# Performance work log

Measured on AMD Instinct MI355X. Metric: run time of the kernel, lower is better.

## Reference

```python
import jax, jax.numpy as jnp
import numpy as np

EMBED = 1024
HEADS = 16
DK = EMBED // HEADS


def setup_inputs() -> dict:
    key = jax.random.key(0)
    ks = jax.random.split(key, 6)
    B, S = 2, 2048
    scale = 1.0 / np.sqrt(EMBED)
    x = jax.random.normal(ks[0], (B, S, EMBED), dtype=jnp.float32)
    Wq = jax.random.normal(ks[1], (EMBED, EMBED), dtype=jnp.float32) * scale
    Wk = jax.random.normal(ks[2], (EMBED, EMBED), dtype=jnp.float32) * scale
    Wv = jax.random.normal(ks[3], (EMBED, EMBED), dtype=jnp.float32) * scale
    Wo = jax.random.normal(ks[4], (EMBED, EMBED), dtype=jnp.float32) * scale
    qw = jnp.zeros((HEADS, 1), dtype=jnp.float32)  # quantum_weight, init quantum_scale=0
    return {"x": x, "Wq": Wq, "Wk": Wk, "Wv": Wv, "Wo": Wo, "qw": qw}


def reference(x, Wq, Wk, Wv, Wo, qw):
    B, S, E = x.shape
    # nn.Linear with no bias: y = x @ W.T; split heads -> [B,H,S,Dk]
    def proj(W):
        return (x @ W.T).reshape(B, S, HEADS, DK).transpose(0, 2, 1, 3)
    q, k, v = proj(Wq), proj(Wk), proj(Wv)
    scores = jnp.einsum('bhsd,bhtd->bhst', q, k) / np.sqrt(DK)
    attn = jax.nn.softmax(scores, axis=-1)  # dropout in eval mode: identity
    classical = jnp.einsum('bhst,bhtd->bhsd', attn, v)
    w = jax.nn.sigmoid(qw)[:, :, None]  # [H,1,1] per-head mixing weight
    out = w * jnp.sin(classical) + (1.0 - w) * classical
    out = out.transpose(0, 2, 1, 3).reshape(B, S, E)
    return out @ Wo.T
```

## Files before the change

kernel.cpp:

```cpp
#include <hip/hip_runtime.h>
#include <math.h>

constexpr int Ec  = 1024;
constexpr int Hc  = 16;
constexpr int DKc = 64;
constexpr int Bc  = 2;
constexpr int Sc  = 2048;
constexpr int Mc  = Bc * Sc;

typedef _Float16 half8 __attribute__((ext_vector_type(8)));
typedef _Float16 half4 __attribute__((ext_vector_type(4)));
typedef float    floatx4 __attribute__((ext_vector_type(4)));

#define MFMA16(a, b, c) __builtin_amdgcn_mfma_f32_16x16x32_f16(a, b, c, 0, 0, 0)

__device__ __forceinline__ void async_lds16(const _Float16* g, _Float16* l)
{
    __builtin_amdgcn_global_load_lds(
        (const __attribute__((address_space(1))) unsigned int*)g,
        (__attribute__((address_space(3))) unsigned int*)l, 16, 0, 0);
}

__global__ __launch_bounds__(256)
void convert_to_h(const float4* __restrict__ x,
                  const float4* __restrict__ wq,
                  const float4* __restrict__ wk,
                  const float4* __restrict__ wv,
                  const float4* __restrict__ wo,
                  half4* __restrict__ dst)
{
    const int i = blockIdx.x * 256 + threadIdx.x;
    const float4* src; int off;
    if      (i < 1048576) { src = x;  off = i; }
    else if (i < 1310720) { src = wq; off = i - 1048576; }
    else if (i < 1572864) { src = wk; off = i - 1310720; }
    else if (i < 1835008) { src = wv; off = i - 1572864; }
    else                  { src = wo; off = i - 1835008; }
    const float4 v = src[off];
    half4 o;
    o.x = (_Float16)v.x; o.y = (_Float16)v.y;
    o.z = (_Float16)v.z; o.w = (_Float16)v.w;
    dst[i] = o;
}

__device__ __forceinline__ void mfma_gemm_core(const _Float16* __restrict__ A,
                                               const _Float16* __restrict__ Bw,
                                               int m0, int n0,
                                               _Float16* As, _Float16* Bs,
                                               floatx4 acc[4][4])
{
    const int tid  = threadIdx.x;
    const int wave = tid >> 6, lane = tid & 63;
    const int l16  = lane & 15, quad = lane >> 4;
    const int wrow = (wave >> 1) * 64, wcol = (wave & 1) * 64;

    const int srow = wave * 32 + (lane >> 2);
    const int kseg = (lane & 3) * 8;
    const _Float16* ga = A  + (size_t)(m0 + srow) * Ec + kseg;
    const _Float16* gb = Bw + (size_t)(n0 + srow) * Ec + kseg;
    _Float16* lA = As + wave * 1024;
    _Float16* lB = Bs + wave * 1024;

    for (int kt = 0; kt < Ec; kt += 32) {
        async_lds16(ga,             lA);
        async_lds16(ga + 16 * Ec,   lA + 512);
        async_lds16(gb,             lB);
        async_lds16(gb + 16 * Ec,   lB + 512);
        ga += 32; gb += 32;
        __syncthreads();

        half8 af[4], bf[4];
#pragma unroll
        for (int i = 0; i < 4; ++i)
            af[i] = *(const half8*)&As[(wrow + i * 16 + l16) * 32 + quad * 8];
#pragma unroll
        for (int j = 0; j < 4; ++j)
            bf[j] = *(const half8*)&Bs[(wcol + j * 16 + l16) * 32 + quad * 8];
#pragma unroll
        for (int i = 0; i < 4; ++i)
#pragma unroll
            for (int j = 0; j < 4; ++j)
                acc[i][j] = MFMA16(af[i], bf[j], acc[i][j]);
        __syncthreads();
    }
}

__global__ __launch_bounds__(256)
void gemm_qkv_mfma(const _Float16* __restrict__ xh,
                   const _Float16* __restrict__ wqh,
                   const _Float16* __restrict__ wkh,
                   const _Float16* __restrict__ wvh,
                   _Float16* __restrict__ Qh,
                   _Float16* __restrict__ Kh,
                   _Float16* __restrict__ VTh)
{
    __shared__ __align__(16) _Float16 As[128 * 32];
    __shared__ __align__(16) _Float16 Bs[128 * 32];
    const int z = blockIdx.z;
    const _Float16* W = (z == 0) ? wqh : (z == 1) ? wkh : wvh;
    const int m0 = blockIdx.y * 128, n0 = blockIdx.x * 128;

    floatx4 acc[4][4] = {};
    mfma_gemm_core(xh, W, m0, n0, As, Bs, acc);

    const int tid  = threadIdx.x;
    const int wave = tid >> 6, lane = tid & 63;
    const int l16  = lane & 15, quad = lane >> 4;
    const int wrow = (wave >> 1) * 64, wcol = (wave & 1) * 64;

    if (z == 2) {
#pragma unroll
        for (int i = 0; i < 4; ++i)
#pragma unroll
            for (int j = 0; j < 4; ++j) {
                const int n = n0 + wcol + j * 16 + l16;
                const int h = n >> 6, d = n & 63;
#pragma unroll
                for (int r = 0; r < 4; ++r) {
                    const int m = m0 + wrow + i * 16 + quad * 4 + r;
                    const int b = m >> 11, s = m & (Sc - 1);
                    VTh[((size_t)((b * Hc + h) * DKc + d)) * Sc + s] =
                        (_Float16)acc[i][j][r];
                }
            }
    } else {
        _Float16* out = (z == 0) ? Qh : Kh;
        const float scale = (z == 0) ? 0.125f : 1.0f;
#pragma unroll
        for (int i = 0; i < 4; ++i)
#pragma unroll
            for (int j = 0; j < 4; ++j) {
                const int n = n0 + wcol + j * 16 + l16;
#pragma unroll
                for (int r = 0; r < 4; ++r) {
                    const int m = m0 + wrow + i * 16 + quad * 4 + r;
                    out[(size_t)m * Ec + n] = (_Float16)(acc[i][j][r] * scale);
                }
            }
    }
}

__global__ __launch_bounds__(256)
void gemm_out_mfma(const _Float16* __restrict__ A,
                   const _Float16* __restrict__ W,
                   float* __restrict__ C)
{
    __shared__ __align__(16) _Float16 As[128 * 32];
    __shared__ __align__(16) _Float16 Bs[64 * 32];
    const int m0 = blockIdx.y * 128, n0 = blockIdx.x * 64;

    const int tid  = threadIdx.x;
    const int wave = tid >> 6, lane = tid & 63;
    const int l16  = lane & 15, quad = lane >> 4;
    const int wrow = (wave >> 1) * 64, wcol = (wave & 1) * 32;

    const int kseg = (lane & 3) * 8;
    const _Float16* ga = A + (size_t)(m0 + wave * 32 + (lane >> 2)) * Ec + kseg;
    const _Float16* gb = W + (size_t)(n0 + wave * 16 + (lane >> 2)) * Ec + kseg;
    _Float16* lA = As + wave * 1024;
    _Float16* lB = Bs + wave * 512;

    floatx4 acc[4][2] = {};

    for (int kt = 0; kt < Ec; kt += 32) {
        async_lds16(ga,           lA);
        async_lds16(ga + 16 * Ec, lA + 512);
        async_lds16(gb,           lB);
        ga += 32; gb += 32;
        __syncthreads();

        half8 af[4], bf[2];
#pragma unroll
        for (int i = 0; i < 4; ++i)
            af[i] = *(const half8*)&As[(wrow + i * 16 + l16) * 32 + quad * 8];
#pragma unroll
        for (int j = 0; j < 2; ++j)
            bf[j] = *(const half8*)&Bs[(wcol + j * 16 + l16) * 32 + quad * 8];
#pragma unroll
        for (int i = 0; i < 4; ++i)
#pragma unroll
            for (int j = 0; j < 2; ++j)
                acc[i][j] = MFMA16(af[i], bf[j], acc[i][j]);
        __syncthreads();
    }

#pragma unroll
    for (int i = 0; i < 4; ++i)
#pragma unroll
        for (int j = 0; j < 2; ++j) {
            const int n = n0 + wcol + j * 16 + l16;
#pragma unroll
            for (int r = 0; r < 4; ++r) {
                const int m = m0 + wrow + i * 16 + quad * 4 + r;
                C[(size_t)m * Ec + n] = acc[i][j][r];
            }
        }
}

__global__ __launch_bounds__(256)
void flash_attn(const _Float16* __restrict__ Qh,
                const _Float16* __restrict__ Kh,
                const _Float16* __restrict__ VTh,
                const float* __restrict__ qw,
                _Float16* __restrict__ Mixh)
{
    constexpr int BM = 128, BN = 64, LDH = 72;
    __shared__ _Float16 Kt[BN][LDH];
    __shared__ _Float16 Vt[DKc][LDH];
    __shared__ _Float16 Ps[BM][LDH];

    const int tid  = threadIdx.x;
    const int wave = tid >> 6, lane = tid & 63;
    const int quad = lane >> 4, l16 = lane & 15;
    const int q0 = blockIdx.x * BM;
    const int bh = blockIdx.y;
    const int h  = bh & (Hc - 1), b = bh >> 4;

    half8 aq[2][2];
#pragma unroll
    for (int u = 0; u < 2; ++u) {
        const _Float16* qp = Qh + (size_t)(b * Sc + q0 + wave * 32 + u * 16 + l16) * Ec
                                + h * DKc + quad * 8;
        aq[u][0] = *(const half8*)qp;
        aq[u][1] = *(const half8*)(qp + 32);
    }

    const int srow = tid >> 2;
    const int sseg = (tid & 3) * 16;
    const _Float16* Kg = Kh + (size_t)(b * Sc + srow) * Ec + h * DKc + sseg;
    const _Float16* Vg = VTh + ((size_t)(bh * DKc + srow)) * Sc + sseg;

    half8 kr0 = *(const half8*)Kg, kr1 = *(const half8*)(Kg + 8);
    half8 vr0 = *(const half8*)Vg, vr1 = *(const half8*)(Vg + 8);
    Kg += (size_t)BN * Ec; Vg += BN;
    *(half8*)&Kt[srow][sseg]     = kr0;
    *(half8*)&Kt[srow][sseg + 8] = kr1;

    floatx4 o[2][4] = {};
    float l_run[2] = {0.f, 0.f};

    for (int n = 0; n < Sc / BN; ++n) {
        __syncthreads();
        *(half8*)&Vt[srow][sseg]     = vr0;
        *(half8*)&Vt[srow][sseg + 8] = vr1;
        const bool more = (n + 1 < Sc / BN);
        if (more) {
            kr0 = *(const half8*)Kg; kr1 = *(const half8*)(Kg + 8);
            vr0 = *(const half8*)Vg; vr1 = *(const half8*)(Vg + 8);
            Kg += (size_t)BN * Ec; Vg += BN;
        }

        floatx4 st[2][4];
#pragma unroll
        for (int i = 0; i < 4; ++i) {
            const half8 ak0 = *(const half8*)&Kt[i * 16 + l16][quad * 8];
            const half8 ak1 = *(const half8*)&Kt[i * 16 + l16][32 + quad * 8];
            const floatx4 z = {0.f, 0.f, 0.f, 0.f};
            st[0][i] = MFMA16(ak1, aq[0][1], MFMA16(ak0, aq[0][0], z));
            st[1][i] = MFMA16(ak1, aq[1][1], MFMA16(ak0, aq[1][0], z));
        }

#pragma unroll
        for (int u = 0; u < 2; ++u) {
            const int prow = wave * 32 + u * 16 + l16;
#pragma unroll
            for (int i = 0; i < 4; ++i) {
                const float p0 = __expf(st[u][i][0]);
                const float p1 = __expf(st[u][i][1]);
                const float p2 = __expf(st[u][i][2]);
                const float p3 = __expf(st[u][i][3]);
                l_run[u] += (p0 + p1) + (p2 + p3);
                half4 pk;
                pk.x = (_Float16)p0; pk.y = (_Float16)p1;
                pk.z = (_Float16)p2; pk.w = (_Float16)p3;
                *(half4*)&Ps[prow][i * 16 + quad * 4] = pk;
            }
        }
        __syncthreads();

        half8 ap[2][2];
#pragma unroll
        for (int u = 0; u < 2; ++u) {
            const _Float16* pp = &Ps[wave * 32 + u * 16 + l16][quad * 8];
            ap[u][0] = *(const half8*)pp;
            ap[u][1] = *(const half8*)(pp + 32);
        }
#pragma unroll
        for (int jd = 0; jd < 4; ++jd) {
            const half8 bv0 = *(const half8*)&Vt[jd * 16 + l16][quad * 8];
            const half8 bv1 = *(const half8*)&Vt[jd * 16 + l16][32 + quad * 8];
#pragma unroll
            for (int u = 0; u < 2; ++u) {
                o[u][jd] = MFMA16(ap[u][0], bv0, o[u][jd]);
                o[u][jd] = MFMA16(ap[u][1], bv1, o[u][jd]);
            }
        }

        if (more) {
            *(half8*)&Kt[srow][sseg]     = kr0;
            *(half8*)&Kt[srow][sseg + 8] = kr1;
        }
    }

    const float wmix = 1.f / (1.f + __expf(-qw[h]));
#pragma unroll
    for (int u = 0; u < 2; ++u) {
        l_run[u] += __shfl_xor(l_run[u], 16);
        l_run[u] += __shfl_xor(l_run[u], 32);
    }
#pragma unroll
    for (int u = 0; u < 2; ++u)
#pragma unroll
        for (int r = 0; r < 4; ++r) {
            const float l = __shfl(l_run[u], (lane & 48) | (quad * 4 + r));
            const float inv = 1.f / l;
            const int m = q0 + wave * 32 + u * 16 + quad * 4 + r;
            _Float16* mp = Mixh + (size_t)(b * Sc + m) * Ec + h * DKc;
#pragma unroll
            for (int jd = 0; jd < 4; ++jd) {
                const float v = o[u][jd][r] * inv;
                mp[jd * 16 + l16] = (_Float16)(wmix * __sinf(v) + (1.f - wmix) * v);
            }
        }
}

extern "C" void kernel_launch(void* const* d_in, const int* in_sizes, int n_in,
                              void* d_out, int out_size, void* d_ws, size_t ws_size,
                              hipStream_t stream)
{
    const float* x  = (const float*)d_in[0];
    const float* Wq = (const float*)d_in[1];
    const float* Wk = (const float*)d_in[2];
    const float* Wv = (const float*)d_in[3];
    const float* Wo = (const float*)d_in[4];
    const float* qw = (const float*)d_in[5];
    float* out = (float*)d_out;

    _Float16* hb   = (_Float16*)d_ws;
    _Float16* xh   = hb;
    _Float16* wqh  = hb + (size_t)4 * 1024 * 1024;
    _Float16* wkh  = hb + (size_t)5 * 1024 * 1024;
    _Float16* wvh  = hb + (size_t)6 * 1024 * 1024;
    _Float16* woh  = hb + (size_t)7 * 1024 * 1024;
    _Float16* Qh   = hb + (size_t)8 * 1024 * 1024;
    _Float16* Kh   = hb + (size_t)12 * 1024 * 1024;
    _Float16* VTh  = hb + (size_t)16 * 1024 * 1024;
    _Float16* mixh = hb + (size_t)20 * 1024 * 1024;

    convert_to_h<<<dim3(8192), dim3(256), 0, stream>>>(
        (const float4*)x, (const float4*)Wq, (const float4*)Wk,
        (const float4*)Wv, (const float4*)Wo, (half4*)hb);

    gemm_qkv_mfma<<<dim3(Ec / 128, Mc / 128, 3), dim3(256), 0, stream>>>(
        xh, wqh, wkh, wvh, Qh, Kh, VTh);

    flash_attn<<<dim3(Sc / 128, Bc * Hc), dim3(256), 0, stream>>>(
        Qh, Kh, VTh, qw, mixh);

    gemm_out_mfma<<<dim3(Ec / 64, Mc / 128), dim3(256), 0, stream>>>(
        mixh, woh, out);
}
```

Measured before the change: 202.9 us.

## Double-buffer LDS tiles in projection GEMMs and vectorize V-transpose stores

Both projection GEMM kernels now use two LDS buffers, issuing the async global-to-LDS loads for the next K tile before computing on the current one. This aims to overlap global memory latency with MFMA work and drops one barrier per iteration. The V-transpose epilogue now packs four consecutive sequence positions into a single half4 store instead of scalar stores. The cost is doubled LDS use per block, which may reduce occupancy. Correctness relies on the async LDS write being complete when the single end-of-iteration barrier is reached.

```diff
diff --git a/kernel.cpp b/kernel.cpp
--- a/kernel.cpp
+++ b/kernel.cpp
@@ -43,11 +43,11 @@
     dst[i] = o;
 }
 
-__device__ __forceinline__ void mfma_gemm_core(const _Float16* __restrict__ A,
-                                               const _Float16* __restrict__ Bw,
-                                               int m0, int n0,
-                                               _Float16* As, _Float16* Bs,
-                                               floatx4 acc[4][4])
+__device__ __forceinline__ void mfma_gemm_db(const _Float16* __restrict__ A,
+                                             const _Float16* __restrict__ Bw,
+                                             int m0, int n0,
+                                             _Float16* As, _Float16* Bs,
+                                             floatx4 acc[4][4])
 {
     const int tid  = threadIdx.x;
     const int wave = tid >> 6, lane = tid & 63;
@@ -58,29 +58,40 @@
     const int kseg = (lane & 3) * 8;
     const _Float16* ga = A  + (size_t)(m0 + srow) * Ec + kseg;
     const _Float16* gb = Bw + (size_t)(n0 + srow) * Ec + kseg;
-    _Float16* lA = As + wave * 1024;
-    _Float16* lB = Bs + wave * 1024;
+
+    async_lds16(ga,           As + wave * 1024);
+    async_lds16(ga + 16 * Ec, As + wave * 1024 + 512);
+    async_lds16(gb,           Bs + wave * 1024);
+    async_lds16(gb + 16 * Ec, Bs + wave * 1024 + 512);
+    ga += 32; gb += 32;
+    __syncthreads();
 
     for (int kt = 0; kt < Ec; kt += 32) {
-        async_lds16(ga,             lA);
-        async_lds16(ga + 16 * Ec,   lA + 512);
-        async_lds16(gb,             lB);
-        async_lds16(gb + 16 * Ec,   lB + 512);
-        ga += 32; gb += 32;
-        __syncthreads();
-
+        const int cb = (kt >> 5) & 1;
+        if (kt + 32 < Ec) {
+            const int nb = cb ^ 1;
+            async_lds16(ga,           As + nb * 4096 + wave * 1024);
+            async_lds16(ga + 16 * Ec, As + nb * 4096 + wave * 1024 + 512);
+            async_lds16(gb,           Bs + nb * 4096 + wave * 1024);
+            async_lds16(gb + 16 * Ec, Bs + nb * 4096 + wave * 1024 + 512);
+            ga += 32; gb += 32;
+        }
+
+        const _Float16* cA = As + cb * 4096;
+        const _Float16* cB = Bs + cb * 4096;
         half8 af[4], bf[4];
 #pragma unroll
         for (int i = 0; i < 4; ++i)
-            af[i] = *(const half8*)&As[(wrow + i * 16 + l16) * 32 + quad * 8];
+            af[i] = *(const half8*)&cA[(wrow + i * 16 + l16) * 32 + quad * 8];
 #pragma unroll
         for (int j = 0; j < 4; ++j)
-            bf[j] = *(const half8*)&Bs[(wcol + j * 16 + l16) * 32 + quad * 8];
+            bf[j] = *(const half8*)&cB[(wcol + j * 16 + l16) * 32 + quad * 8];
 #pragma unroll
         for (int i = 0; i < 4; ++i)
 #pragma unroll
             for (int j = 0; j < 4; ++j)
                 acc[i][j] = MFMA16(af[i], bf[j], acc[i][j]);
+
         __syncthreads();
     }
 }
@@ -94,14 +105,14 @@
                    _Float16* __restrict__ Kh,
                    _Float16* __restrict__ VTh)
 {
-    __shared__ __align__(16) _Float16 As[128 * 32];
-    __shared__ __align__(16) _Float16 Bs[128 * 32];
+    __shared__ __align__(16) _Float16 As[2 * 128 * 32];
+    __shared__ __align__(16) _Float16 Bs[2 * 128 * 32];
     const int z = blockIdx.z;
     const _Float16* W = (z == 0) ? wqh : (z == 1) ? wkh : wvh;
     const int m0 = blockIdx.y * 128, n0 = blockIdx.x * 128;
 
     floatx4 acc[4][4] = {};
-    mfma_gemm_core(xh, W, m0, n0, As, Bs, acc);
+    mfma_gemm_db(xh, W, m0, n0, As, Bs, acc);
 
     const int tid  = threadIdx.x;
     const int wave = tid >> 6, lane = tid & 63;
@@ -113,15 +124,14 @@
         for (int i = 0; i < 4; ++i)
 #pragma unroll
             for (int j = 0; j < 4; ++j) {
-                const int n = n0 + wcol + j * 16 + l16;
-                const int h = n >> 6, d = n & 63;
-#pragma unroll
-                for (int r = 0; r < 4; ++r) {
-                    const int m = m0 + wrow + i * 16 + quad * 4 + r;
-                    const int b = m >> 11, s = m & (Sc - 1);
-                    VTh[((size_t)((b * Hc + h) * DKc + d)) * Sc + s] =
-                        (_Float16)acc[i][j][r];
-                }
+                const int n  = n0 + wcol + j * 16 + l16;
+                const int hh = n >> 6, d = n & 63;
+                const int mb = m0 + wrow + i * 16 + quad * 4;
+                const int bb = mb >> 11, s = mb & (Sc - 1);
+                half4 pk;
+#pragma unroll
+                for (int r = 0; r < 4; ++r) pk[r] = (_Float16)acc[i][j][r];
+                *(half4*)&VTh[((size_t)((bb * Hc + hh) * DKc + d)) * Sc + s] = pk;
             }
     } else {
         _Float16* out = (z == 0) ? Qh : Kh;
@@ -145,8 +155,8 @@
                    const _Float16* __restrict__ W,
                    float* __restrict__ C)
 {
-    __shared__ __align__(16) _Float16 As[128 * 32];
-    __shared__ __align__(16) _Float16 Bs[64 * 32];
+    __shared__ __align__(16) _Float16 As[2 * 128 * 32];
+    __shared__ __align__(16) _Float16 Bs[2 * 64 * 32];
     const int m0 = blockIdx.y * 128, n0 = blockIdx.x * 64;
 
     const int tid  = threadIdx.x;
@@ -154,33 +164,44 @@
     const int l16  = lane & 15, quad = lane >> 4;
     const int wrow = (wave >> 1) * 64, wcol = (wave & 1) * 32;
 
+    const int srow = lane >> 2;
     const int kseg = (lane & 3) * 8;
-    const _Float16* ga = A + (size_t)(m0 + wave * 32 + (lane >> 2)) * Ec + kseg;
-    const _Float16* gb = W + (size_t)(n0 + wave * 16 + (lane >> 2)) * Ec + kseg;
-    _Float16* lA = As + wave * 1024;
-    _Float16* lB = Bs + wave * 512;
+    const _Float16* ga = A + (size_t)(m0 + wave * 32 + srow) * Ec + kseg;
+    const _Float16* gb = W + (size_t)(n0 + wave * 16 + (srow & 15)) * Ec + kseg;
 
     floatx4 acc[4][2] = {};
 
+    async_lds16(ga,           As + wave * 1024);
+    async_lds16(ga + 16 * Ec, As + wave * 1024 + 512);
+    async_lds16(gb,           Bs + wave * 512);
+    ga += 32; gb += 32;
+    __syncthreads();
+
     for (int kt = 0; kt < Ec; kt += 32) {
-        async_lds16(ga,           lA);
-        async_lds16(ga + 16 * Ec, lA + 512);
-        async_lds16(gb,           lB);
-        ga += 32; gb += 32;
-        __syncthreads();
-
+        const int cb = (kt >> 5) & 1;
+        if (kt + 32 < Ec) {
+            const int nb = cb ^ 1;
+            async_lds16(ga,           As + nb * 4096 + wave * 1024);
+            async_lds16(ga + 16 * Ec, As + nb * 4096 + wave * 1024 + 512);
+            async_lds16(gb,           Bs + nb * 2048 + wave * 512);
+            ga += 32; gb += 32;
+        }
+
+        const _Float16* cA = As + cb * 4096;
+        const _Float16* cB = Bs + cb * 2048;
         half8 af[4], bf[2];
 #pragma unroll
         for (int i = 0; i < 4; ++i)
-            af[i] = *(const half8*)&As[(wrow + i * 16 + l16) * 32 + quad * 8];
+            af[i] = *(const half8*)&cA[(wrow + i * 16 + l16) * 32 + quad * 8];
 #pragma unroll
         for (int j = 0; j < 2; ++j)
-            bf[j] = *(const half8*)&Bs[(wcol + j * 16 + l16) * 32 + quad * 8];
+            bf[j] = *(const half8*)&cB[(wcol + j * 16 + l16) * 32 + quad * 8];
 #pragma unroll
         for (int i = 0; i < 4; ++i)
 #pragma unroll
             for (int j = 0; j < 2; ++j)
                 acc[i][j] = MFMA16(af[i], bf[j], acc[i][j]);
+
         __syncthreads();
     }
 
```

Result: faster. 194.8 us (-4.0%).
